# Performance work log

Measured on AMD Instinct MI355X. Metric: run time of the kernel, lower is better.

Reference implementation:

```python
import jax, jax.numpy as jnp
import numpy as np

N = 129  # fixed by fc1: 3*121 -> N-8 = 121
F = 262144
E = 16384

def setup_inputs() -> dict:
    key = jax.random.key(0)
    ks = jax.random.split(key, 18)
    s = 0.05
    return {
        "x": jax.random.normal(ks[0], (N, F), jnp.float32),
        "edge_index": jax.random.randint(ks[1], (2, E), 0, N),
        "edge_attr": jax.random.uniform(ks[2], (E, 3), jnp.float32),
        # GCNConvSortPool (channel1 only; forward reuses it for all 3 edge channels)
        "gcn1_W": jax.random.normal(ks[3], (F, 1), jnp.float32) * (1.0 / np.sqrt(F)),
        "gcn1_b": jnp.zeros((1,), jnp.float32),
        "gcn2_W": jax.random.normal(ks[4], (1, 1), jnp.float32),
        "gcn2_b": jnp.zeros((1,), jnp.float32),
        "conv1_w": jax.random.normal(ks[5], (3, 2, 3), jnp.float32) * s,  # OIH
        "conv1_b": jax.random.normal(ks[6], (3,), jnp.float32) * s,
        "conv2_w": jax.random.normal(ks[7], (1, 3, 3), jnp.float32) * s,
        "conv2_b": jax.random.normal(ks[8], (1,), jnp.float32) * s,
        "fc1_W": jax.random.normal(ks[9], (3 * 121, 32), jnp.float32) * s,
        "fc1_b": jnp.zeros((32,), jnp.float32),
        "fc2_W": jax.random.normal(ks[10], (32, 6), jnp.float32) * s,
        "fc2_b": jnp.zeros((6,), jnp.float32),
        "fc3_W": jax.random.normal(ks[11], (6, 2), jnp.float32) * s,
        "fc3_b": jnp.zeros((2,), jnp.float32),
    }

def _gcn_conv(x, row, col, ew, W, b):
    # PyG GCNConv with edge weights: add self loops (weight 1), symmetric norm.
    n = x.shape[0]
    xw = x @ W                                             # [n, out]
    loop = jnp.arange(n)
    row2 = jnp.concatenate([row, loop])
    col2 = jnp.concatenate([col, loop])
    ew2 = jnp.concatenate([ew, jnp.ones((n,), x.dtype)])
    deg = jax.ops.segment_sum(ew2, col2, num_segments=n)
    dinv = jnp.where(deg > 0, deg ** -0.5, 0.0)
    norm = dinv[row2] * ew2 * dinv[col2]                   # [e+n]
    out = jax.ops.segment_sum(norm[:, None] * xw[row2], col2, num_segments=n)
    return out + b

def _maxpool1d3(z):
    return jax.lax.reduce_window(z, -jnp.inf, jax.lax.max, (1, 1, 3), (1, 1, 1), 'VALID')

def _conv1d(z, w, b):
    out = jax.lax.conv_general_dilated(z, w, (1,), 'VALID', dimension_numbers=('NCH', 'OIH', 'NCH'))
    return out + b[None, :, None]

def _channel(x, row, col, ew, gcn1_W, gcn1_b, gcn2_W, gcn2_b, conv1_w, conv1_b, conv2_w, conv2_b):
    h1 = _gcn_conv(x, row, col, ew, gcn1_W, gcn1_b)        # [N,1]
    h2 = _gcn_conv(h1[:, -1:], row, col, ew, gcn2_W, gcn2_b)  # [N,1]
    h = jnp.concatenate([h1, h2], axis=-1)                 # [N,2]
    perm = jnp.argsort(-h[:, -1])                          # SortPool: sort by last channel, descending, k=N
    h = h[perm]                                            # [N,2]
    z = h.T[None]                                          # [1,2,N]
    z = _maxpool1d3(_conv1d(z, conv1_w, conv1_b))          # [1,3,N-4]
    z = _maxpool1d3(_conv1d(z, conv2_w, conv2_b))          # [1,1,N-8]
    return z

def reference(x, edge_index, edge_attr, gcn1_W, gcn1_b, gcn2_W, gcn2_b,
              conv1_w, conv1_b, conv2_w, conv2_b,
              fc1_W, fc1_b, fc2_W, fc2_b, fc3_W, fc3_b):
    row, col = edge_index[0], edge_index[1]
    outs = [_channel(x, row, col, edge_attr[:, c], gcn1_W, gcn1_b, gcn2_W, gcn2_b,
                     conv1_w, conv1_b, conv2_w, conv2_b) for c in range(3)]
    all_x = jnp.concatenate(outs, axis=-2)                 # [1,3,121]
    h = all_x.reshape(1, -1)                               # [1,363]
    h = jax.nn.elu(h @ fc1_W + fc1_b)                      # dropout=0 -> identity
    h = jax.nn.elu(h @ fc2_W + fc2_b)
    return h @ fc3_W + fc3_b                               # [1,2]
```

## Files before the change

kernel.cpp:

```cpp
#include <hip/hip_runtime.h>
#include <hip/hip_bf16.h>
#include <math.h>

#define NN 129
#define FF 262144
#define EE 16384
#define CHUNKS 32
#define CHUNK (FF / CHUNKS)
#define NB 16
#define EPB (EE / NB)
#define EPT (EPB / 256)

#define OFF_PARTIAL 0
#define OFF_DEGP    (OFF_PARTIAL + NN*CHUNKS)
#define OFF_H1P     (OFF_DEGP + NB*3*NN)
#define OFF_H2P     (OFF_H1P + NB*3*NN)
#define OFF_BAR     (OFF_H2P + NB*3*NN)

typedef float vfloat4 __attribute__((ext_vector_type(4)));

__global__ __launch_bounds__(256) void k_matvec(
    const float* __restrict__ x, const float* __restrict__ W,
    const int* __restrict__ eidx, const float* __restrict__ eattr,
    double* __restrict__ ws)
{
    const int b = blockIdx.x;
    const int tid = threadIdx.x;
    const int wave = tid >> 6, lane = tid & 63;

    __shared__ double ws4[4];
    __shared__ double dp[4][3][NN];

    if (b < NN * CHUNKS) {
        const int r = b / CHUNKS, ch = b % CHUNKS;
        const vfloat4* xp = (const vfloat4*)(x + (size_t)r * FF + (size_t)ch * CHUNK);
        const float4*  wp = (const float4*)(W + (size_t)ch * CHUNK);
        double acc0 = 0.0, acc1 = 0.0;
#pragma unroll
        for (int i = 0; i < CHUNK / (256 * 4); ++i) {
            vfloat4 xv = __builtin_nontemporal_load(xp + tid + i * 256);
            float4  wv = wp[tid + i * 256];
            acc0 += (double)xv[0] * (double)wv.x + (double)xv[1] * (double)wv.y;
            acc1 += (double)xv[2] * (double)wv.z + (double)xv[3] * (double)wv.w;
        }
        double acc = acc0 + acc1;
        for (int off = 32; off > 0; off >>= 1) acc += __shfl_down(acc, off, 64);
        if (lane == 0) ws4[wave] = acc;
        __syncthreads();
        if (tid == 0) ws[OFF_PARTIAL + b] = (ws4[0] + ws4[1]) + (ws4[2] + ws4[3]);
    } else {
        const int bb = b - NN * CHUNKS;
        if (bb == 0 && tid == 0) {
            unsigned* bar = (unsigned*)(ws + OFF_BAR);
            __hip_atomic_store(&bar[0], 0u, __ATOMIC_RELAXED, __HIP_MEMORY_SCOPE_AGENT);
            __hip_atomic_store(&bar[1], 0u, __ATOMIC_RELAXED, __HIP_MEMORY_SCOPE_AGENT);
        }
        for (int i = tid; i < 4 * 3 * NN; i += 256) ((double*)dp)[i] = 0.0;
        __syncthreads();
        const int* col = eidx + EE;
#pragma unroll
        for (int i = 0; i < EPT; ++i) {
            const int e = bb * EPB + i * 256 + tid;
            const int cl = col[e];
#pragma unroll
            for (int c = 0; c < 3; ++c)
                unsafeAtomicAdd(&dp[wave][c][cl], (double)eattr[e * 3 + c]);
        }
        __syncthreads();
        for (int i = tid; i < 3 * NN; i += 256) {
            const int c = i / NN, j = i % NN;
            ws[OFF_DEGP + bb * (3 * NN) + i] =
                (dp[0][c][j] + dp[1][c][j]) + (dp[2][c][j] + dp[3][c][j]);
        }
    }
}

__device__ __forceinline__ void gbar(unsigned* bar, int idx) {
    __syncthreads();
    if (threadIdx.x == 0) {
        __threadfence();
        __hip_atomic_fetch_add(&bar[idx], 1u, __ATOMIC_ACQ_REL, __HIP_MEMORY_SCOPE_AGENT);
        while (__hip_atomic_load(&bar[idx], __ATOMIC_ACQUIRE, __HIP_MEMORY_SCOPE_AGENT) < (unsigned)NB)
            __builtin_amdgcn_s_sleep(1);
        __threadfence();
    }
    __syncthreads();
}

__global__ __launch_bounds__(256) void k_rest(
    const int* __restrict__ eidx, const float* __restrict__ eattr,
    double* __restrict__ ws,
    const float* __restrict__ b1, const float* __restrict__ W2, const float* __restrict__ b2,
    const float* __restrict__ c1w, const float* __restrict__ c1b,
    const float* __restrict__ c2w, const float* __restrict__ c2b,
    const float* __restrict__ f1W, const float* __restrict__ f1b,
    const float* __restrict__ f2W, const float* __restrict__ f2b,
    const float* __restrict__ f3W, const float* __restrict__ f3b,
    float* __restrict__ out)
{
    __shared__ double sxw[NN];
    __shared__ double sdinv[3][NN];
    __shared__ double sh1[3][NN];
    __shared__ double hp[4][3][NN];
    __shared__ double h2f[3][NN];
    __shared__ double z0[3][NN], z1[3][NN];
    __shared__ int    rnk[3][NN];
    __shared__ double c1o[3][3][127];
    __shared__ double p1o[3][3][125];
    __shared__ double c2o[3][123];
    __shared__ double allx[363];
    __shared__ double fc1o[32], fc2o[6];

    const int b = blockIdx.x, tid = threadIdx.x, wave = tid >> 6;
    unsigned* bar = (unsigned*)(ws + OFF_BAR);

    int er[EPT], ec[EPT];
    float ea[EPT][3];
#pragma unroll
    for (int i = 0; i < EPT; ++i) {
        const int e = b * EPB + i * 256 + tid;
        er[i] = eidx[e];
        ec[i] = eidx[EE + e];
        ea[i][0] = eattr[e * 3 + 0];
        ea[i][1] = eattr[e * 3 + 1];
        ea[i][2] = eattr[e * 3 + 2];
    }

    for (int j = tid; j < NN; j += 256) {
        double s = 0.0;
#pragma unroll
        for (int k = 0; k < CHUNKS; ++k) s += ws[OFF_PARTIAL + j * CHUNKS + k];
        sxw[j] = s;
    }
    for (int v = tid; v < 3 * NN; v += 256) {
        double d = 1.0;
#pragma unroll
        for (int k = 0; k < NB; ++k) d += ws[OFF_DEGP + k * (3 * NN) + v];
        ((double*)sdinv)[v] = (d > 0.0) ? 1.0 / sqrt(d) : 0.0;
    }
    for (int i = tid; i < 4 * 3 * NN; i += 256) ((double*)hp)[i] = 0.0;
    __syncthreads();

    double enw[EPT][3];
#pragma unroll
    for (int i = 0; i < EPT; ++i) {
        const int r = er[i], cl = ec[i];
        const double xwr = sxw[r];
#pragma unroll
        for (int c = 0; c < 3; ++c) {
            const double nw = sdinv[c][r] * (double)ea[i][c] * sdinv[c][cl];
            enw[i][c] = nw;
            unsafeAtomicAdd(&hp[wave][c][cl], nw * xwr);
        }
    }
    __syncthreads();
    for (int i = tid; i < 3 * NN; i += 256) {
        const int c = i / NN, j = i % NN;
        ws[OFF_H1P + b * (3 * NN) + i] =
            (hp[0][c][j] + hp[1][c][j]) + (hp[2][c][j] + hp[3][c][j]);
    }
    gbar(bar, 0);

    const double bb1 = (double)b1[0];
    for (int i = tid; i < 3 * NN; i += 256) {
        const int j = i % NN;
        const double dv = ((double*)sdinv)[i];
        double s = dv * dv * sxw[j] + bb1;
#pragma unroll
        for (int k = 0; k < NB; ++k) s += ws[OFF_H1P + k * (3 * NN) + i];
        ((double*)sh1)[i] = s;
    }
    for (int i = tid; i < 4 * 3 * NN; i += 256) ((double*)hp)[i] = 0.0;
    __syncthreads();

    const double w2 = (double)W2[0];
#pragma unroll
    for (int i = 0; i < EPT; ++i) {
        const int r = er[i], cl = ec[i];
#pragma unroll
        for (int c = 0; c < 3; ++c)
            unsafeAtomicAdd(&hp[wave][c][cl], enw[i][c] * (sh1[c][r] * w2));
    }
    __syncthreads();
    for (int i = tid; i < 3 * NN; i += 256) {
        const int c = i / NN, j = i % NN;
        ws[OFF_H2P + b * (3 * NN) + i] =
            (hp[0][c][j] + hp[1][c][j]) + (hp[2][c][j] + hp[3][c][j]);
    }
    gbar(bar, 1);

    if (b != 0) return;

    const double bb2 = (double)b2[0];
    for (int i = tid; i < 3 * NN; i += 256) {
        const int j = i % NN;
        const double dv = ((double*)sdinv)[i];
        double s = dv * dv * (((double*)sh1)[i] * w2) + bb2;
#pragma unroll
        for (int k = 0; k < NB; ++k) s += ws[OFF_H2P + k * (3 * NN) + i];
        ((double*)h2f)[i] = s;
    }
    __syncthreads();

    for (int i = tid; i < 3 * NN; i += 256) {
        const int c = i / NN, j = i % NN;
        const double v = h2f[c][j];
        int rk = 0;
        for (int q = 0; q < NN; ++q) {
            const double u = h2f[c][q];
            rk += (u > v) || (u == v && q < j);
        }
        rnk[c][j] = rk;
    }
    __syncthreads();
    for (int i = tid; i < 3 * NN; i += 256) {
        const int c = i / NN, j = i % NN;
        const int rk = rnk[c][j];
        z0[c][rk] = sh1[c][j];
        z1[c][rk] = h2f[c][j];
    }
    __syncthreads();

    for (int i = tid; i < 3 * 3 * 127; i += 256) {
        const int c = i / (3 * 127), rem = i % (3 * 127), o = rem / 127, p = rem % 127;
        double s = (double)c1b[o];
#pragma unroll
        for (int k = 0; k < 3; ++k) {
            s += (double)c1w[(o * 2 + 0) * 3 + k] * z0[c][p + k];
            s += (double)c1w[(o * 2 + 1) * 3 + k] * z1[c][p + k];
        }
        c1o[c][o][p] = s;
    }
    __syncthreads();
    for (int i = tid; i < 3 * 3 * 125; i += 256) {
        const int c = i / (3 * 125), rem = i % (3 * 125), o = rem / 125, p = rem % 125;
        p1o[c][o][p] = fmax(c1o[c][o][p], fmax(c1o[c][o][p + 1], c1o[c][o][p + 2]));
    }
    __syncthreads();
    for (int i = tid; i < 3 * 123; i += 256) {
        const int c = i / 123, p = i % 123;
        double s = (double)c2b[0];
#pragma unroll
        for (int ic = 0; ic < 3; ++ic)
#pragma unroll
            for (int k = 0; k < 3; ++k)
                s += (double)c2w[ic * 3 + k] * p1o[c][ic][p + k];
        c2o[c][p] = s;
    }
    __syncthreads();
    for (int i = tid; i < 3 * 121; i += 256) {
        const int c = i / 121, p = i % 121;
        allx[c * 121 + p] = fmax(c2o[c][p], fmax(c2o[c][p + 1], c2o[c][p + 2]));
    }
    __syncthreads();

    {
        const int j = tid >> 3, t = tid & 7;
        double s = 0.0;
        for (int i = t; i < 363; i += 8) s += allx[i] * (double)f1W[i * 32 + j];
        s += __shfl_down(s, 4, 8);
        s += __shfl_down(s, 2, 8);
        s += __shfl_down(s, 1, 8);
        if (t == 0) {
            s += (double)f1b[j];
            fc1o[j] = (s > 0.0) ? s : expm1(s);
        }
    }
    __syncthreads();
    if (tid < 6) {
        double s = (double)f2b[tid];
        for (int i = 0; i < 32; ++i) s += fc1o[i] * (double)f2W[i * 6 + tid];
        fc2o[tid] = (s > 0.0) ? s : expm1(s);
    }
    __syncthreads();
    if (tid < 2) {
        double s = (double)f3b[tid];
        for (int i = 0; i < 6; ++i) s += fc2o[i] * (double)f3W[i * 2 + tid];
        out[tid] = (float)s;
    }
}

extern "C" void kernel_launch(void* const* d_in, const int* in_sizes, int n_in,
                              void* d_out, int out_size, void* d_ws, size_t ws_size,
                              hipStream_t stream) {
    const float* x    = (const float*)d_in[0];
    const int*   eidx = (const int*)d_in[1];
    const float* eattr= (const float*)d_in[2];
    const float* g1W  = (const float*)d_in[3];
    const float* g1b  = (const float*)d_in[4];
    const float* g2W  = (const float*)d_in[5];
    const float* g2b  = (const float*)d_in[6];
    const float* c1w  = (const float*)d_in[7];
    const float* c1b  = (const float*)d_in[8];
    const float* c2w  = (const float*)d_in[9];
    const float* c2b  = (const float*)d_in[10];
    const float* f1W  = (const float*)d_in[11];
    const float* f1b  = (const float*)d_in[12];
    const float* f2W  = (const float*)d_in[13];
    const float* f2b  = (const float*)d_in[14];
    const float* f3W  = (const float*)d_in[15];
    const float* f3b  = (const float*)d_in[16];
    float* out = (float*)d_out;
    double* ws = (double*)d_ws;

    k_matvec<<<NN * CHUNKS + NB, 256, 0, stream>>>(x, g1W, eidx, eattr, ws);
    k_rest<<<NB, 256, 0, stream>>>(eidx, eattr, ws,
                                   g1b, g2W, g2b, c1w, c1b, c2w, c2b,
                                   f1W, f1b, f2W, f2b, f3W, f3b, out);
}
```

Measured before the change: 257.1 us.

## Fuse matvec and graph stages into one kernel with atomic completion counter

Merges the two kernel launches into a single persistent kernel. The first 16 blocks handle degree computation and the GCN/tail stages, and the remaining blocks do the x@W matvec and signal completion through an atomic counter. The graph blocks compute degrees while the matvec streams, then spin until all matvec partials arrive, removing one launch and its gap. It adds a memset launch for the counters and relies on the 16 low-index blocks being co-resident with the matvec blocks. Shared-memory buffers are also aliased and the first maxpool is folded into conv2.

Result: slower. 625.0 us (+143.1%).

```diff
diff --git a/kernel.cpp b/kernel.cpp
--- a/kernel.cpp
+++ b/kernel.cpp
@@ -19,75 +19,20 @@
 
 typedef float vfloat4 __attribute__((ext_vector_type(4)));
 
-__global__ __launch_bounds__(256) void k_matvec(
-    const float* __restrict__ x, const float* __restrict__ W,
-    const int* __restrict__ eidx, const float* __restrict__ eattr,
-    double* __restrict__ ws)
-{
-    const int b = blockIdx.x;
-    const int tid = threadIdx.x;
-    const int wave = tid >> 6, lane = tid & 63;
-
-    __shared__ double ws4[4];
-    __shared__ double dp[4][3][NN];
-
-    if (b < NN * CHUNKS) {
-        const int r = b / CHUNKS, ch = b % CHUNKS;
-        const vfloat4* xp = (const vfloat4*)(x + (size_t)r * FF + (size_t)ch * CHUNK);
-        const float4*  wp = (const float4*)(W + (size_t)ch * CHUNK);
-        double acc0 = 0.0, acc1 = 0.0;
-#pragma unroll
-        for (int i = 0; i < CHUNK / (256 * 4); ++i) {
-            vfloat4 xv = __builtin_nontemporal_load(xp + tid + i * 256);
-            float4  wv = wp[tid + i * 256];
-            acc0 += (double)xv[0] * (double)wv.x + (double)xv[1] * (double)wv.y;
-            acc1 += (double)xv[2] * (double)wv.z + (double)xv[3] * (double)wv.w;
-        }
-        double acc = acc0 + acc1;
-        for (int off = 32; off > 0; off >>= 1) acc += __shfl_down(acc, off, 64);
-        if (lane == 0) ws4[wave] = acc;
-        __syncthreads();
-        if (tid == 0) ws[OFF_PARTIAL + b] = (ws4[0] + ws4[1]) + (ws4[2] + ws4[3]);
-    } else {
-        const int bb = b - NN * CHUNKS;
-        if (bb == 0 && tid == 0) {
-            unsigned* bar = (unsigned*)(ws + OFF_BAR);
-            __hip_atomic_store(&bar[0], 0u, __ATOMIC_RELAXED, __HIP_MEMORY_SCOPE_AGENT);
-            __hip_atomic_store(&bar[1], 0u, __ATOMIC_RELAXED, __HIP_MEMORY_SCOPE_AGENT);
-        }
-        for (int i = tid; i < 4 * 3 * NN; i += 256) ((double*)dp)[i] = 0.0;
-        __syncthreads();
-        const int* col = eidx + EE;
-#pragma unroll
-        for (int i = 0; i < EPT; ++i) {
-            const int e = bb * EPB + i * 256 + tid;
-            const int cl = col[e];
-#pragma unroll
-            for (int c = 0; c < 3; ++c)
-                unsafeAtomicAdd(&dp[wave][c][cl], (double)eattr[e * 3 + c]);
-        }
-        __syncthreads();
-        for (int i = tid; i < 3 * NN; i += 256) {
-            const int c = i / NN, j = i % NN;
-            ws[OFF_DEGP + bb * (3 * NN) + i] =
-                (dp[0][c][j] + dp[1][c][j]) + (dp[2][c][j] + dp[3][c][j]);
-        }
-    }
-}
-
-__device__ __forceinline__ void gbar(unsigned* bar, int idx) {
+__device__ __forceinline__ void gbar(unsigned* cnt, int idx) {
     __syncthreads();
     if (threadIdx.x == 0) {
         __threadfence();
-        __hip_atomic_fetch_add(&bar[idx], 1u, __ATOMIC_ACQ_REL, __HIP_MEMORY_SCOPE_AGENT);
-        while (__hip_atomic_load(&bar[idx], __ATOMIC_ACQUIRE, __HIP_MEMORY_SCOPE_AGENT) < (unsigned)NB)
+        __hip_atomic_fetch_add(&cnt[idx], 1u, __ATOMIC_ACQ_REL, __HIP_MEMORY_SCOPE_AGENT);
+        while (__hip_atomic_load(&cnt[idx], __ATOMIC_ACQUIRE, __HIP_MEMORY_SCOPE_AGENT) < (unsigned)NB)
             __builtin_amdgcn_s_sleep(1);
         __threadfence();
     }
     __syncthreads();
 }
 
-__global__ __launch_bounds__(256) void k_rest(
+__global__ __launch_bounds__(256) void k_fused(
+    const float* __restrict__ x, const float* __restrict__ W,
     const int* __restrict__ eidx, const float* __restrict__ eattr,
     double* __restrict__ ws,
     const float* __restrict__ b1, const float* __restrict__ W2, const float* __restrict__ b2,
@@ -98,21 +43,46 @@
     const float* __restrict__ f3W, const float* __restrict__ f3b,
     float* __restrict__ out)
 {
-    __shared__ double sxw[NN];
-    __shared__ double sdinv[3][NN];
-    __shared__ double sh1[3][NN];
-    __shared__ double hp[4][3][NN];
-    __shared__ double h2f[3][NN];
-    __shared__ double z0[3][NN], z1[3][NN];
-    __shared__ int    rnk[3][NN];
-    __shared__ double c1o[3][3][127];
-    __shared__ double p1o[3][3][125];
-    __shared__ double c2o[3][123];
-    __shared__ double allx[363];
-    __shared__ double fc1o[32], fc2o[6];
-
-    const int b = blockIdx.x, tid = threadIdx.x, wave = tid >> 6;
-    unsigned* bar = (unsigned*)(ws + OFF_BAR);
+    const int b = blockIdx.x;
+    const int tid = threadIdx.x;
+    const int wave = tid >> 6, lane = tid & 63;
+
+    __shared__ double P[129 + 387 + 387];
+    __shared__ double SCR[1917];
+    __shared__ double ws4[4];
+    __shared__ double fcb[38];
+
+    unsigned* cnt = (unsigned*)(ws + OFF_BAR);
+
+    if (b >= NB) {
+        const int bm = b - NB;
+        const int r = bm / CHUNKS, ch = bm % CHUNKS;
+        const vfloat4* xp = (const vfloat4*)(x + (size_t)r * FF + (size_t)ch * CHUNK);
+        const float4*  wp = (const float4*)(W + (size_t)ch * CHUNK);
+        double acc0 = 0.0, acc1 = 0.0;
+#pragma unroll
+        for (int i = 0; i < CHUNK / (256 * 4); ++i) {
+            vfloat4 xv = __builtin_nontemporal_load(xp + tid + i * 256);
+            float4  wv = wp[tid + i * 256];
+            acc0 += (double)xv[0] * (double)wv.x + (double)xv[1] * (double)wv.y;
+            acc1 += (double)xv[2] * (double)wv.z + (double)xv[3] * (double)wv.w;
+        }
+        double acc = acc0 + acc1;
+        for (int off = 32; off > 0; off >>= 1) acc += __shfl_down(acc, off, 64);
+        if (lane == 0) ws4[wave] = acc;
+        __syncthreads();
+        if (tid == 0) {
+            ws[OFF_PARTIAL + bm] = (ws4[0] + ws4[1]) + (ws4[2] + ws4[3]);
+            __threadfence();
+            __hip_atomic_fetch_add(&cnt[0], 1u, __ATOMIC_ACQ_REL, __HIP_MEMORY_SCOPE_AGENT);
+        }
+        return;
+    }
+
+    double* sxw   = P;
+    double* sdinv = P + 129;
+    double* sh1   = P + 516;
+    double (*hp)[3][NN] = (double(*)[3][NN])SCR;
 
     int er[EPT], ec[EPT];
     float ea[EPT][3];
@@ -126,17 +96,44 @@
         ea[i][2] = eattr[e * 3 + 2];
     }
 
+    for (int i = tid; i < 4 * 3 * NN; i += 256) ((double*)hp)[i] = 0.0;
+    __syncthreads();
+#pragma unroll
+    for (int i = 0; i < EPT; ++i) {
+        const int cl = ec[i];
+#pragma unroll
+        for (int c = 0; c < 3; ++c)
+            unsafeAtomicAdd(&hp[wave][c][cl], (double)ea[i][c]);
+    }
+    __syncthreads();
+    for (int i = tid; i < 3 * NN; i += 256) {
+        const int c = i / NN, j = i % NN;
+        ws[OFF_DEGP + b * (3 * NN) + i] =
+            (hp[0][c][j] + hp[1][c][j]) + (hp[2][c][j] + hp[3][c][j]);
+    }
+    gbar(cnt, 1);
+
+    for (int v = tid; v < 3 * NN; v += 256) {
+        double d = 1.0;
+#pragma unroll
+        for (int k = 0; k < NB; ++k) d += ws[OFF_DEGP + k * (3 * NN) + v];
+        sdinv[v] = (d > 0.0) ? 1.0 / sqrt(d) : 0.0;
+    }
+
+    __syncthreads();
+    if (tid == 0) {
+        while (__hip_atomic_load(&cnt[0], __ATOMIC_ACQUIRE, __HIP_MEMORY_SCOPE_AGENT)
+               < (unsigned)(NN * CHUNKS))
+            __builtin_amdgcn_s_sleep(1);
+        __threadfence();
+    }
+    __syncthreads();
+
     for (int j = tid; j < NN; j += 256) {
         double s = 0.0;
 #pragma unroll
         for (int k = 0; k < CHUNKS; ++k) s += ws[OFF_PARTIAL + j * CHUNKS + k];
         sxw[j] = s;
-    }
-    for (int v = tid; v < 3 * NN; v += 256) {
-        double d = 1.0;
-#pragma unroll
-        for (int k = 0; k < NB; ++k) d += ws[OFF_DEGP + k * (3 * NN) + v];
-        ((double*)sdinv)[v] = (d > 0.0) ? 1.0 / sqrt(d) : 0.0;
     }
     for (int i = tid; i < 4 * 3 * NN; i += 256) ((double*)hp)[i] = 0.0;
     __syncthreads();
@@ -148,7 +145,7 @@
         const double xwr = sxw[r];
 #pragma unroll
         for (int c = 0; c < 3; ++c) {
-            const double nw = sdinv[c][r] * (double)ea[i][c] * sdinv[c][cl];
+            const double nw = sdinv[c * NN + r] * (double)ea[i][c] * sdinv[c * NN + cl];
             enw[i][c] = nw;
             unsafeAtomicAdd(&hp[wave][c][cl], nw * xwr);
         }
@@ -159,16 +156,16 @@
         ws[OFF_H1P + b * (3 * NN) + i] =
             (hp[0][c][j] + hp[1][c][j]) + (hp[2][c][j] + hp[3][c][j]);
     }
-    gbar(bar, 0);
+    gbar(cnt, 2);
 
     const double bb1 = (double)b1[0];
     for (int i = tid; i < 3 * NN; i += 256) {
         const int j = i % NN;
-        const double dv = ((double*)sdinv)[i];
+        const double dv = sdinv[i];
         double s = dv * dv * sxw[j] + bb1;
 #pragma unroll
         for (int k = 0; k < NB; ++k) s += ws[OFF_H1P + k * (3 * NN) + i];
-        ((double*)sh1)[i] = s;
+        sh1[i] = s;
     }
     for (int i = tid; i < 4 * 3 * NN; i += 256) ((double*)hp)[i] = 0.0;
     __syncthreads();
@@ -179,7 +176,7 @@
         const int r = er[i], cl = ec[i];
 #pragma unroll
         for (int c = 0; c < 3; ++c)
-            unsafeAtomicAdd(&hp[wave][c][cl], enw[i][c] * (sh1[c][r] * w2));
+            unsafeAtomicAdd(&hp[wave][c][cl], enw[i][c] * (sh1[c * NN + r] * w2));
     }
     __syncthreads();
     for (int i = tid; i < 3 * NN; i += 256) {
@@ -187,37 +184,47 @@
         ws[OFF_H2P + b * (3 * NN) + i] =
             (hp[0][c][j] + hp[1][c][j]) + (hp[2][c][j] + hp[3][c][j]);
     }
-    gbar(bar, 1);
+    gbar(cnt, 3);
 
     if (b != 0) return;
 
+    double* z0   = SCR;
+    double* z1   = SCR + 387;
+    double* c1o  = SCR + 774;
+    double* h2f  = SCR + 1161;
+    int*    rnk  = (int*)(SCR + 1548);
+    double* c2o  = SCR;
+    double* allx = SCR + 369;
+    double* fc1o = fcb;
+    double* fc2o = fcb + 32;
+
     const double bb2 = (double)b2[0];
     for (int i = tid; i < 3 * NN; i += 256) {
         const int j = i % NN;
-        const double dv = ((double*)sdinv)[i];
-        double s = dv * dv * (((double*)sh1)[i] * w2) + bb2;
+        const double dv = sdinv[i];
+        double s = dv * dv * (sh1[i] * w2) + bb2;
 #pragma unroll
         for (int k = 0; k < NB; ++k) s += ws[OFF_H2P + k * (3 * NN) + i];
-        ((double*)h2f)[i] = s;
+        h2f[i] = s;
     }
     __syncthreads();
 
     for (int i = tid; i < 3 * NN; i += 256) {
         const int c = i / NN, j = i % NN;
-        const double v = h2f[c][j];
+        const double v = h2f[c * NN + j];
         int rk = 0;
         for (int q = 0; q < NN; ++q) {
-            const double u = h2f[c][q];
+            const double u = h2f[c * NN + q];
             rk += (u > v) || (u == v && q < j);
         }
-        rnk[c][j] = rk;
-    }
-    __syncthreads();
-    for (int i = tid; i < 3 * NN; i += 256) {
-        const int c = i / NN, j = i % NN;
-        const int rk = rnk[c][j];
-        z0[c][rk] = sh1[c][j];
-        z1[c][rk] = h2f[c][j];
+        rnk[i] = rk;
+    }
+    __syncthreads();
+    for (int i = tid; i < 3 * NN; i += 256) {
+        const int c = i / NN;
+        const int rk = rnk[i];
+        z0[c * NN + rk] = sh1[i];
+        z1[c * NN + rk] = h2f[i];
     }
     __syncthreads();
 
@@ -226,31 +233,31 @@
         double s = (double)c1b[o];
 #pragma unroll
         for (int k = 0; k < 3; ++k) {
-            s += (double)c1w[(o * 2 + 0) * 3 + k] * z0[c][p + k];
-            s += (double)c1w[(o * 2 + 1) * 3 + k] * z1[c][p + k];
-        }
-        c1o[c][o][p] = s;
-    }
-    __syncthreads();
-    for (int i = tid; i < 3 * 3 * 125; i += 256) {
-        const int c = i / (3 * 125), rem = i % (3 * 125), o = rem / 125, p = rem % 125;
-        p1o[c][o][p] = fmax(c1o[c][o][p], fmax(c1o[c][o][p + 1], c1o[c][o][p + 2]));
-    }
-    __syncthreads();
+            s += (double)c1w[(o * 2 + 0) * 3 + k] * z0[c * NN + p + k];
+            s += (double)c1w[(o * 2 + 1) * 3 + k] * z1[c * NN + p + k];
+        }
+        c1o[(c * 3 + o) * 127 + p] = s;
+    }
+    __syncthreads();
+
     for (int i = tid; i < 3 * 123; i += 256) {
         const int c = i / 123, p = i % 123;
         double s = (double)c2b[0];
 #pragma unroll
         for (int ic = 0; ic < 3; ++ic)
 #pragma unroll
-            for (int k = 0; k < 3; ++k)
-                s += (double)c2w[ic * 3 + k] * p1o[c][ic][p + k];
-        c2o[c][p] = s;
+            for (int k = 0; k < 3; ++k) {
+                const double* base = c1o + (c * 3 + ic) * 127 + p + k;
+                const double m = fmax(base[0], fmax(base[1], base[2]));
+                s += (double)c2w[ic * 3 + k] * m;
+            }
+        c2o[c * 123 + p] = s;
     }
     __syncthreads();
     for (int i = tid; i < 3 * 121; i += 256) {
         const int c = i / 121, p = i % 121;
-        allx[c * 121 + p] = fmax(c2o[c][p], fmax(c2o[c][p + 1], c2o[c][p + 2]));
+        allx[c * 121 + p] = fmax(c2o[c * 123 + p],
+                            fmax(c2o[c * 123 + p + 1], c2o[c * 123 + p + 2]));
     }
     __syncthreads();
 
@@ -303,8 +310,9 @@
     float* out = (float*)d_out;
     double* ws = (double*)d_ws;
 
-    k_matvec<<<NN * CHUNKS + NB, 256, 0, stream>>>(x, g1W, eidx, eattr, ws);
-    k_rest<<<NB, 256, 0, stream>>>(eidx, eattr, ws,
-                                   g1b, g2W, g2b, c1w, c1b, c2w, c2b,
-                                   f1W, f1b, f2W, f2b, f3W, f3b, out);
+    hipMemsetAsync((void*)(ws + OFF_BAR), 0, 4 * sizeof(unsigned), stream);
+    k_fused<<<NN * CHUNKS + NB, 256, 0, stream>>>(
+        x, g1W, eidx, eattr, ws,
+        g1b, g2W, g2b, c1w, c1b, c2w, c2b,
+        f1W, f1b, f2W, f2b, f3W, f3b, out);
 }
```
